# Optimization experiments

Hardware: AMD Instinct MI355X
Metric: run time of the kernel (lower is better)

Reference implementation:

```python
import jax, jax.numpy as jnp
import numpy as np

B, N, DEG = 16, 2048, 16          # graphs, nodes per graph, avg out-degree
C_IN, HID, K = 64, 128, 32        # in_channels, hidden_channels, out_channels (clusters)
NT = B * N                        # total nodes
E = NT * DEG                      # total edges
GN_EPS = 1e-5


def setup_inputs() -> dict:
    key = jax.random.key(0)
    ks = jax.random.split(key, 6)
    x = jax.random.normal(ks[0], (NT, C_IN), jnp.float32)
    # within-graph random edges (sorted batch => node i belongs to graph i // N)
    src_l = jax.random.randint(ks[1], (E,), 0, N)
    dst_l = jax.random.randint(ks[2], (E,), 0, N)
    gid = jnp.repeat(jnp.arange(B, dtype=jnp.int32), N * DEG)
    edge_index = jnp.stack([gid * N + src_l, gid * N + dst_l]).astype(jnp.int32)
    batch = jnp.repeat(jnp.arange(B, dtype=jnp.int32), N)
    return dict(
        x=x, edge_index=edge_index, batch=batch,
        gn_weight=jnp.ones((C_IN,), jnp.float32),
        gn_bias=jnp.zeros((C_IN,), jnp.float32),
        gn_mean_scale=jnp.ones((C_IN,), jnp.float32),
        w1=jax.random.normal(ks[3], (C_IN, HID), jnp.float32) / np.float32(np.sqrt(C_IN)),
        b1=jnp.zeros((HID,), jnp.float32),
        w2=jax.random.normal(ks[4], (HID, K), jnp.float32) / np.float32(np.sqrt(HID)),
        b2=jnp.zeros((K,), jnp.float32),
    )


def reference(x, gn_weight, gn_bias, gn_mean_scale, w1, b1, w2, b2, edge_index, batch):
    # ---- GraphNorm (per-graph mean/var with learnable mean scale) ----
    ones_n = jnp.ones((NT,), x.dtype)
    cnt = jax.ops.segment_sum(ones_n, batch, num_segments=B)[:, None]        # [B,1]
    mean = jax.ops.segment_sum(x, batch, num_segments=B) / cnt              # [B,C]
    xm = x - gn_mean_scale * mean[batch]
    var = jax.ops.segment_sum(xm * xm, batch, num_segments=B) / cnt         # [B,C]
    h = gn_weight * xm / jnp.sqrt(var + GN_EPS)[batch] + gn_bias            # [NT,C_IN]

    # ---- GCNConv (add self-loops, symmetric D^-1/2 (A+I) D^-1/2) ----
    src, dst = edge_index[0], edge_index[1]
    loop = jnp.arange(NT, dtype=src.dtype)
    src_l = jnp.concatenate([src, loop])
    dst_l = jnp.concatenate([dst, loop])
    deg = jax.ops.segment_sum(jnp.ones_like(src_l, x.dtype), dst_l, num_segments=NT)
    dinv = jnp.where(deg > 0, jax.lax.rsqrt(deg), 0.0)
    norm = dinv[src_l] * dinv[dst_l]                                        # [E+NT]
    hw = h @ w1                                                             # [NT,HID]
    h = jax.ops.segment_sum(norm[:, None] * hw[src_l], dst_l, num_segments=NT) + b1
    h = jax.nn.selu(h)

    # ---- to_dense_batch / to_dense_adj (uniform graph sizes -> mask all True) ----
    xd = h.reshape(B, N, HID)                                               # [B,N,F]
    adj = jnp.zeros((B, N, N), x.dtype).at[batch[src], src % N, dst % N].add(1.0)

    # ---- DMoNPooling ----
    s = jax.nn.softmax(xd @ w2 + b2, axis=-1)                               # [B,N,K]
    out = jax.nn.selu(jnp.einsum('bnk,bnf->bkf', s, xd))                    # [B,K,F]
    sta = jnp.einsum('bnk,bnm->bkm', s, adj)                                # [B,K,N]
    out_adj = jnp.einsum('bkm,bml->bkl', sta, s)                            # [B,K,K]

    degrees = adj.sum(-1)                                                   # [B,N]
    m = degrees.sum(-1) / 2                                                 # [B]
    ca = jnp.einsum('bnk,bn->bk', s, degrees)                               # [B,K]
    normalizer = ca[:, :, None] * ca[:, None, :] / 2 / m[:, None, None]
    spectral_loss = (-jnp.einsum('bkk->b', out_adj - normalizer) / (2 * m)).mean()

    ss = jnp.einsum('bnk,bnl->bkl', s, s)                                   # [B,K,K]
    ss_fro = jnp.sqrt(jnp.sum(ss * ss, axis=(-2, -1), keepdims=True))
    eye = jnp.eye(K, dtype=x.dtype)
    diff = ss / ss_fro - eye / jnp.sqrt(jnp.float32(K))
    ortho_loss = jnp.sqrt(jnp.sum(diff * diff, axis=(-2, -1))).mean()

    cluster_size = s.sum(1)                                                 # [B,K]
    cluster_loss = (jnp.linalg.norm(cluster_size, axis=1) / N
                    * jnp.sqrt(jnp.float32(K)) - 1).mean()
    # (coarsened-adj renormalization in DMoNPooling is unused by Net's outputs)

    return jax.nn.log_softmax(out, axis=-1), spectral_loss + ortho_loss + cluster_loss, s
```

## Files before the change

### kernel.cpp

```cpp
#include <hip/hip_runtime.h>
#include <cmath>

static constexpr int B_  = 16;
static constexpr int N_  = 2048;
static constexpr int NT_ = 32768;
static constexpr int E_  = 524288;

static constexpr size_t OFF_HSC    = 0;
static constexpr size_t OFF_XD     = 2097152;
static constexpr size_t OFF_SWS    = 6291456;
static constexpr size_t OFF_PART   = 7340032;
static constexpr size_t OFF_DINV   = 8388608;
static constexpr size_t OFF_SHIFT  = 8421376;
static constexpr size_t OFF_SCALE  = 8422400;
static constexpr size_t OFF_GSP    = 8423424;
static constexpr size_t OFF_GSP2   = 8431616;
static constexpr size_t OFF_SSP    = 8439808;
static constexpr size_t OFF_CAP    = 8701952;
static constexpr size_t OFF_CSP    = 8710144;
static constexpr size_t OFF_SPECP  = 8718336;
static constexpr size_t OFF_ICNTO  = 8718592;
static constexpr size_t OFF_IROWS  = 8751360;
static constexpr size_t OFF_IESRC  = 8784132;

__device__ __forceinline__ float selu_f(float x) {
  return 1.0507009873554805f * (x > 0.f ? x : 1.6732632423543772f * expm1f(x));
}

__device__ __forceinline__ float block_sum_bcast(float v, float* sm) {
  int lane = threadIdx.x & 63, w = threadIdx.x >> 6;
#pragma unroll
  for (int off = 32; off; off >>= 1) v += __shfl_down(v, off);
  __syncthreads();
  if (lane == 0) sm[w] = v;
  __syncthreads();
  return sm[0] + sm[1] + sm[2] + sm[3];
}

__global__ __launch_bounds__(1024) void k_graph(const int* ei, const float* x,
                                                int* rows, int* esrc, int* cout_,
                                                float* dinv, float* gsp, float* gsp2) {
  __shared__ int hin[2048], hout[2048], sb[1024];
  __shared__ float l1[16][64], l2[16][64];
  int blk = blockIdx.x;
  int tid = threadIdx.x;
  if (blk < 16) {
    int g = blk;
    int nbase = g * 2048;
    int ebase = g * 32768;
    hin[tid] = 0; hin[tid + 1024] = 0;
    hout[tid] = 0; hout[tid + 1024] = 0;
    __syncthreads();
    for (int i = tid; i < 32768; i += 1024) {
      int s = ei[ebase + i];
      int d = ei[E_ + ebase + i];
      atomicAdd(&hout[s - nbase], 1);
      atomicAdd(&hin[d - nbase], 1);
    }
    __syncthreads();
    int a = hin[2 * tid], b2 = hin[2 * tid + 1];
    sb[tid] = a + b2;
    __syncthreads();
    for (int off = 1; off < 1024; off <<= 1) {
      int add = (tid >= off) ? sb[tid - off] : 0;
      __syncthreads();
      sb[tid] += add;
      __syncthreads();
    }
    int pref = (tid > 0) ? sb[tid - 1] : 0;
    int r0 = ebase + pref, r1 = r0 + a;
    int n0 = nbase + 2 * tid;
    rows[n0] = r0; rows[n0 + 1] = r1;
    dinv[n0] = rsqrtf((float)(a + 1));
    dinv[n0 + 1] = rsqrtf((float)(b2 + 1));
    cout_[n0] = hout[2 * tid];
    cout_[n0 + 1] = hout[2 * tid + 1];
    if (blk == 15 && tid == 1023) rows[NT_] = E_;
    __syncthreads();
    hin[2 * tid] = r0; hin[2 * tid + 1] = r1;
    __syncthreads();
    for (int i = tid; i < 32768; i += 1024) {
      int s = ei[ebase + i];
      int d = ei[E_ + ebase + i];
      int pos = atomicAdd(&hin[d - nbase], 1);
      esrc[pos] = s;
    }
  } else {
    int gi = blk - 16;
    int b = gi >> 3, chunk = gi & 7;
    int c = tid & 63, r = tid >> 6;
    float s = 0.f, s2 = 0.f;
    const float* xb = x + ((size_t)b * N_ + (size_t)chunk * 256) * 64;
    for (int n = r; n < 256; n += 16) {
      float v = xb[n * 64 + c];
      s += v; s2 += v * v;
    }
    l1[r][c] = s; l2[r][c] = s2;
    __syncthreads();
    if (r == 0) {
      float t1 = 0.f, t2 = 0.f;
#pragma unroll
      for (int i = 0; i < 16; i++) { t1 += l1[i][c]; t2 += l2[i][c]; }
      gsp[gi * 64 + c] = t1;
      gsp2[gi * 64 + c] = t2;
    }
  }
}

__global__ __launch_bounds__(1024) void k_fin(const float* gsp, const float* gsp2,
                                              const float* gw, const float* gms,
                                              float* shift, float* scalev, float* lossp) {
  int t = threadIdx.x;
  int b = t >> 6, c = t & 63;
  float s = 0.f, s2 = 0.f;
#pragma unroll
  for (int chunk = 0; chunk < 8; chunk++) {
    s  += gsp[(b * 8 + chunk) * 64 + c];
    s2 += gsp2[(b * 8 + chunk) * 64 + c];
  }
  float mean = s * (1.f / 2048.f);
  float a = gms[c];
  float var = s2 * (1.f / 2048.f) - (2.f * a - a * a) * mean * mean;
  shift[t] = a * mean;
  scalev[t] = gw[c] * rsqrtf(var + 1e-5f);
  if (t == 0) lossp[0] = 0.f;
}

__global__ void k_prep(const float* x, const float* shift, const float* scalev,
                       const float* gb, const float* dinv, float* hsc) {
  int idx = blockIdx.x * 256 + threadIdx.x;
  int node = idx >> 4, g4 = (idx & 15) * 4;
  int b = node >> 11;
  float di = dinv[node];
  float4 xv = *(const float4*)&x[(size_t)node * 64 + g4];
  float4 sh = *(const float4*)&shift[b * 64 + g4];
  float4 sc = *(const float4*)&scalev[b * 64 + g4];
  float4 bb = *(const float4*)&gb[g4];
  float4 o;
  o.x = ((xv.x - sh.x) * sc.x + bb.x) * di;
  o.y = ((xv.y - sh.y) * sc.y + bb.y) * di;
  o.z = ((xv.z - sh.z) * sc.z + bb.z) * di;
  o.w = ((xv.w - sh.w) * sc.w + bb.w) * di;
  *(float4*)&hsc[(size_t)node * 64 + g4] = o;
}

__global__ __launch_bounds__(256) void k_mm1(const float* hsc, const float* dinv,
                                             const int* rows, const int* esrc,
                                             const float* w1, const float* b1,
                                             float* xd) {
  __shared__ float at[32 * 65];
  int tid = threadIdx.x;
  int n0 = blockIdx.x * 32;
  int wv = tid >> 6, c = tid & 63;
  for (int i = 0; i < 8; i++) {
    int nn = i * 4 + wv;
    int node = n0 + nn;
    int e0 = rows[node], e1 = rows[node + 1];
    float dd = dinv[node];
    float acc = hsc[(size_t)node * 64 + c];
    for (int e = e0; e < e1; e += 8) {
      int sidx[8]; float wt[8], hv[8];
#pragma unroll
      for (int j = 0; j < 8; j++) {
        int ee = e + j;
        sidx[j] = esrc[ee < e1 ? ee : e0];
        wt[j] = (ee < e1) ? 1.f : 0.f;
      }
#pragma unroll
      for (int j = 0; j < 8; j++) hv[j] = hsc[(size_t)sidx[j] * 64 + c];
#pragma unroll
      for (int j = 0; j < 8; j++) acc += wt[j] * hv[j];
    }
    at[nn * 65 + c] = dd * acc;
  }
  __syncthreads();
  int tx = tid & 31, ty = tid >> 5;
  int f0 = tx * 4, nn = ty * 4;
  float acc[4][4] = {};
  for (int k = 0; k < 64; k++) {
    float4 wvv = *(const float4*)&w1[k * 128 + f0];
#pragma unroll
    for (int i = 0; i < 4; i++) {
      float av = at[(nn + i) * 65 + k];
      acc[i][0] += av * wvv.x; acc[i][1] += av * wvv.y;
      acc[i][2] += av * wvv.z; acc[i][3] += av * wvv.w;
    }
  }
  float4 bv = *(const float4*)&b1[f0];
#pragma unroll
  for (int i = 0; i < 4; i++) {
    float4 o;
    o.x = selu_f(acc[i][0] + bv.x);
    o.y = selu_f(acc[i][1] + bv.y);
    o.z = selu_f(acc[i][2] + bv.z);
    o.w = selu_f(acc[i][3] + bv.w);
    *(float4*)&xd[(size_t)(n0 + nn + i) * 128 + f0] = o;
  }
}

__global__ __launch_bounds__(256) void k_mm2s(const float* xd, const float* w2,
                                              const float* b2, float* s_ws,
                                              float* outs) {
  __shared__ float w2s[128 * 32];
  __shared__ float xt[64 * 129];
  __shared__ float lg[64 * 33];
  int tid = threadIdx.x;
  for (int i = tid; i < 4096; i += 256) w2s[i] = w2[i];
  int n0 = blockIdx.x * 64;
  for (int i = tid; i < 2048; i += 256) {
    int n = i >> 5, j4 = (i & 31) * 4;
    float4 v = *(const float4*)&xd[(size_t)(n0 + n) * 128 + j4];
    xt[n * 129 + j4] = v.x; xt[n * 129 + j4 + 1] = v.y;
    xt[n * 129 + j4 + 2] = v.z; xt[n * 129 + j4 + 3] = v.w;
  }
  __syncthreads();
  int ty = tid >> 3;
  int k0 = (tid & 7) * 4;
  float acc[2][4] = {};
  for (int j = 0; j < 128; j++) {
    float4 wv = *(float4*)&w2s[j * 32 + k0];
    float x0 = xt[(ty * 2) * 129 + j];
    float x1 = xt[(ty * 2 + 1) * 129 + j];
    acc[0][0] += x0 * wv.x; acc[0][1] += x0 * wv.y; acc[0][2] += x0 * wv.z; acc[0][3] += x0 * wv.w;
    acc[1][0] += x1 * wv.x; acc[1][1] += x1 * wv.y; acc[1][2] += x1 * wv.z; acc[1][3] += x1 * wv.w;
  }
  float4 bv = *(const float4*)&b2[k0];
#pragma unroll
  for (int i = 0; i < 2; i++) {
    int n = ty * 2 + i;
    lg[n * 33 + k0]     = acc[i][0] + bv.x;
    lg[n * 33 + k0 + 1] = acc[i][1] + bv.y;
    lg[n * 33 + k0 + 2] = acc[i][2] + bv.z;
    lg[n * 33 + k0 + 3] = acc[i][3] + bv.w;
  }
  __syncthreads();
  if (tid < 64) {
    float m = -3.4e38f;
    for (int kk = 0; kk < 32; kk++) m = fmaxf(m, lg[tid * 33 + kk]);
    float ssum = 0.f;
    for (int kk = 0; kk < 32; kk++) {
      float e = expf(lg[tid * 33 + kk] - m);
      lg[tid * 33 + kk] = e; ssum += e;
    }
    float inv = 1.f / ssum;
    for (int k4 = 0; k4 < 32; k4 += 4) {
      float4 o;
      o.x = lg[tid * 33 + k4] * inv;     o.y = lg[tid * 33 + k4 + 1] * inv;
      o.z = lg[tid * 33 + k4 + 2] * inv; o.w = lg[tid * 33 + k4 + 3] * inv;
      *(float4*)&s_ws[(size_t)(n0 + tid) * 32 + k4] = o;
      float* op = &outs[(size_t)(n0 + tid) * 32 + k4];
      op[0] = o.x; op[1] = o.y; op[2] = o.z; op[3] = o.w;
    }
  }
}

__global__ __launch_bounds__(256) void k_stats(const float* s_ws, const int* cout_,
    const int* ei, float* ssp, float* cap, float* csp, float* specp) {
  __shared__ float st[128 * 33];
  __shared__ float r1[8][32], r2[8][32];
  __shared__ float sm4[4];
  int blk = blockIdx.x;
  int b = blk >> 4, chunk = blk & 15;
  int tid = threadIdx.x;
  int nbase = b * 2048 + chunk * 128;
  for (int i = tid; i < 4096; i += 256) {
    int n = i >> 5, kk = i & 31;
    st[n * 33 + kk] = s_ws[(size_t)(nbase + n) * 32 + kk];
  }
  __syncthreads();
  int k = tid >> 3, l0 = (tid & 7) * 4;
  float a0 = 0, a1 = 0, a2 = 0, a3 = 0;
  for (int n = 0; n < 128; n++) {
    float sk = st[n * 33 + k];
    a0 += sk * st[n * 33 + l0];     a1 += sk * st[n * 33 + l0 + 1];
    a2 += sk * st[n * 33 + l0 + 2]; a3 += sk * st[n * 33 + l0 + 3];
  }
  float4 o = {a0, a1, a2, a3};
  *(float4*)&ssp[(size_t)blk * 1024 + k * 32 + l0] = o;
  int k2 = tid & 31, r = tid >> 5;
  float aca = 0.f, acs = 0.f;
  for (int i = 0; i < 16; i++) {
    int n = i * 8 + r;
    float dg = (float)cout_[nbase + n];
    float v = st[n * 33 + k2];
    acs += v; aca += v * dg;
  }
  r1[r][k2] = aca; r2[r][k2] = acs;
  __syncthreads();
  if (r == 0) {
    float sa = 0.f, sc = 0.f;
#pragma unroll
    for (int i = 0; i < 8; i++) { sa += r1[i][k2]; sc += r2[i][k2]; }
    cap[blk * 32 + k2] = sa;
    csp[blk * 32 + k2] = sc;
  }
  int ebase = b * 32768 + chunk * 2048;
  float acc = 0.f;
  for (int j = 0; j < 8; j++) {
    int e = ebase + j * 256 + tid;
    int s = ei[e], d = ei[E_ + e];
    const float4* ap = (const float4*)&s_ws[(size_t)s * 32];
    const float4* cp = (const float4*)&s_ws[(size_t)d * 32];
#pragma unroll
    for (int q = 0; q < 8; q++) {
      float4 u = ap[q], v = cp[q];
      acc += u.x * v.x + u.y * v.y + u.z * v.z + u.w * v.w;
    }
  }
  int lane = tid & 63, w = tid >> 6;
#pragma unroll
  for (int off = 32; off; off >>= 1) acc += __shfl_down(acc, off);
  __syncthreads();
  if (lane == 0) sm4[w] = acc;
  __syncthreads();
  if (tid == 0) specp[blk] = sm4[0] + sm4[1] + sm4[2] + sm4[3];
}

__global__ __launch_bounds__(256) void k_outp(const float* s_ws, const float* xd,
                                              float* partial) {
  __shared__ float st[64 * 36];
  __shared__ float xt[64 * 132];
  int b = blockIdx.x & 15, chunk = blockIdx.x >> 4;
  int tid = threadIdx.x;
  int tx = tid & 31, ty = tid >> 5;
  int f0 = tx * 4, k0 = ty * 4;
  float acc[4][4] = {};
  for (int sub = 0; sub < 2; sub++) {
    int base = b * 2048 + chunk * 128 + sub * 64;
    __syncthreads();
    for (int i = tid; i < 2048; i += 256) {
      int n = i >> 5, kk = i & 31;
      st[n * 36 + kk] = s_ws[(size_t)(base + n) * 32 + kk];
    }
    for (int i = tid; i < 8192; i += 256) {
      int n = i >> 7, j = i & 127;
      xt[n * 132 + j] = xd[(size_t)(base + n) * 128 + j];
    }
    __syncthreads();
    for (int n = 0; n < 64; n++) {
      float4 sv = *(float4*)&st[n * 36 + k0];
      float4 xv = *(float4*)&xt[n * 132 + f0];
      acc[0][0] += sv.x * xv.x; acc[0][1] += sv.x * xv.y; acc[0][2] += sv.x * xv.z; acc[0][3] += sv.x * xv.w;
      acc[1][0] += sv.y * xv.x; acc[1][1] += sv.y * xv.y; acc[1][2] += sv.y * xv.z; acc[1][3] += sv.y * xv.w;
      acc[2][0] += sv.z * xv.x; acc[2][1] += sv.z * xv.y; acc[2][2] += sv.z * xv.z; acc[2][3] += sv.z * xv.w;
      acc[3][0] += sv.w * xv.x; acc[3][1] += sv.w * xv.y; acc[3][2] += sv.w * xv.z; acc[3][3] += sv.w * xv.w;
    }
  }
  int pbase = (chunk * 16 + b) * 32;
#pragma unroll
  for (int i = 0; i < 4; i++) {
    float4 o = {acc[i][0], acc[i][1], acc[i][2], acc[i][3]};
    *(float4*)&partial[(size_t)(pbase + k0 + i) * 128 + f0] = o;
  }
}

__global__ void k_outf(const float* partial, float* out0) {
  int row = blockIdx.x;
  int b = row >> 5, k = row & 31;
  int f = threadIdx.x;
  float v = 0.f;
#pragma unroll
  for (int c = 0; c < 16; c++) v += partial[(size_t)(((c * 16 + b) * 32 + k)) * 128 + f];
  v = selu_f(v);
  int lane = threadIdx.x & 63, w = threadIdx.x >> 6;
  __shared__ float s1[2], s2[2];
  float m = v;
#pragma unroll
  for (int off = 32; off; off >>= 1) m = fmaxf(m, __shfl_down(m, off));
  if (lane == 0) s1[w] = m;
  __syncthreads();
  m = fmaxf(s1[0], s1[1]);
  float e = expf(v - m), t = e;
#pragma unroll
  for (int off = 32; off; off >>= 1) t += __shfl_down(t, off);
  if (lane == 0) s2[w] = t;
  __syncthreads();
  float tot = s2[0] + s2[1];
  out0[(size_t)row * 128 + f] = v - m - logf(tot);
}

__global__ void k_loss(const float* ssp, const float* csp, const float* cap,
                       const float* specp, float* loss) {
  int b = blockIdx.x;
  __shared__ float sm[4];
  int tid = threadIdx.x;
  float v0 = 0, v1 = 0, v2 = 0, v3 = 0;
  for (int c = 0; c < 16; c++) {
    float4 u = *(const float4*)&ssp[(size_t)(b * 16 + c) * 1024 + tid * 4];
    v0 += u.x; v1 += u.y; v2 += u.z; v3 += u.w;
  }
  float ssq = v0 * v0 + v1 * v1 + v2 * v2 + v3 * v3;
  ssq = block_sum_bcast(ssq, sm);
  float inv = 1.f / sqrtf(ssq);
  float dsq = 0.f;
  {
    int i0 = tid * 4;
    float vv[4] = {v0, v1, v2, v3};
#pragma unroll
    for (int j = 0; j < 4; j++) {
      int i = i0 + j;
      float d = vv[j] * inv;
      if ((i >> 5) == (i & 31)) d -= 0.17677669529663687f;
      dsq += d * d;
    }
  }
  dsq = block_sum_bcast(dsq, sm);
  float csq = 0.f, casq = 0.f;
  if (tid < 32) {
    float c1 = 0.f, c2 = 0.f;
    for (int c = 0; c < 16; c++) {
      c1 += csp[(size_t)(b * 16 + c) * 32 + tid];
      c2 += cap[(size_t)(b * 16 + c) * 32 + tid];
    }
    csq = c1 * c1; casq = c2 * c2;
  }
  csq = block_sum_bcast(csq, sm);
  casq = block_sum_bcast(casq, sm);
  float spec_sum = (tid < 16) ? specp[b * 16 + tid] : 0.f;
  spec_sum = block_sum_bcast(spec_sum, sm);
  if (tid == 0) {
    float ortho = sqrtf(dsq);
    float cl = sqrtf(csq) * (1.f / 2048.f) * 5.656854249492381f - 1.f;
    float m = 16384.f;
    float spec = -(spec_sum - casq / (2.f * m)) / (2.f * m);
    atomicAdd(loss, (spec + ortho + cl) * (1.f / 16.f));
  }
}

extern "C" void kernel_launch(void* const* d_in, const int* in_sizes, int n_in,
                              void* d_out, int out_size, void* d_ws, size_t ws_size,
                              hipStream_t stream) {
  (void)in_sizes; (void)n_in; (void)out_size; (void)ws_size;
  const float* x   = (const float*)d_in[0];
  const int*   ei  = (const int*)d_in[1];
  const float* gw  = (const float*)d_in[3];
  const float* gb  = (const float*)d_in[4];
  const float* gms = (const float*)d_in[5];
  const float* w1  = (const float*)d_in[6];
  const float* b1  = (const float*)d_in[7];
  const float* w2  = (const float*)d_in[8];
  const float* b2  = (const float*)d_in[9];
  float* out = (float*)d_out;
  float* ws  = (float*)d_ws;

  float* hsc    = ws + OFF_HSC;
  float* xd     = ws + OFF_XD;
  float* s_ws   = ws + OFF_SWS;
  float* part   = ws + OFF_PART;
  float* dinv   = ws + OFF_DINV;
  float* shift  = ws + OFF_SHIFT;
  float* scalev = ws + OFF_SCALE;
  float* gsp    = ws + OFF_GSP;
  float* gsp2   = ws + OFF_GSP2;
  float* ssp    = ws + OFF_SSP;
  float* cap    = ws + OFF_CAP;
  float* csp    = ws + OFF_CSP;
  float* specp  = ws + OFF_SPECP;
  int*   cout_  = (int*)(ws + OFF_ICNTO);
  int*   rows   = (int*)(ws + OFF_IROWS);
  int*   esrc   = (int*)(ws + OFF_IESRC);

  float* out0  = out;
  float* lossp = out + 65536;
  float* outs  = out + 65537;

  hipLaunchKernelGGL(k_graph, dim3(144), dim3(1024), 0, stream,
                     ei, x, rows, esrc, cout_, dinv, gsp, gsp2);
  hipLaunchKernelGGL(k_fin, dim3(1), dim3(1024), 0, stream,
                     gsp, gsp2, gw, gms, shift, scalev, lossp);
  hipLaunchKernelGGL(k_prep, dim3(2048), dim3(256), 0, stream,
                     x, shift, scalev, gb, dinv, hsc);
  hipLaunchKernelGGL(k_mm1, dim3(1024), dim3(256), 0, stream, hsc, dinv, rows, esrc, w1, b1, xd);
  hipLaunchKernelGGL(k_mm2s, dim3(512), dim3(256), 0, stream, xd, w2, b2, s_ws, outs);
  hipLaunchKernelGGL(k_stats, dim3(256), dim3(256), 0, stream, s_ws, cout_, ei, ssp, cap, csp, specp);
  hipLaunchKernelGGL(k_outp, dim3(256), dim3(256), 0, stream, s_ws, xd, part);
  hipLaunchKernelGGL(k_outf, dim3(512), dim3(128), 0, stream, part, out0);
  hipLaunchKernelGGL(k_loss, dim3(16), dim3(256), 0, stream, ssp, csp, cap, specp, lossp);
}
```

Measured before the change: 214.9 us.

## Fuse softmax, cluster stats and pooled output into mm2; fold GraphNorm finalize into prep

```diff
diff --git a/kernel.cpp b/kernel.cpp
--- a/kernel.cpp
+++ b/kernel.cpp
@@ -10,18 +10,16 @@
 static constexpr size_t OFF_XD     = 2097152;
 static constexpr size_t OFF_SWS    = 6291456;
 static constexpr size_t OFF_PART   = 7340032;
-static constexpr size_t OFF_DINV   = 8388608;
-static constexpr size_t OFF_SHIFT  = 8421376;
-static constexpr size_t OFF_SCALE  = 8422400;
-static constexpr size_t OFF_GSP    = 8423424;
-static constexpr size_t OFF_GSP2   = 8431616;
-static constexpr size_t OFF_SSP    = 8439808;
-static constexpr size_t OFF_CAP    = 8701952;
-static constexpr size_t OFF_CSP    = 8710144;
-static constexpr size_t OFF_SPECP  = 8718336;
-static constexpr size_t OFF_ICNTO  = 8718592;
-static constexpr size_t OFF_IROWS  = 8751360;
-static constexpr size_t OFF_IESRC  = 8784132;
+static constexpr size_t OFF_DINV   = 9437184;
+static constexpr size_t OFF_GSP    = 9469952;
+static constexpr size_t OFF_GSP2   = 9478144;
+static constexpr size_t OFF_SSP    = 9486336;
+static constexpr size_t OFF_CAP    = 10010624;
+static constexpr size_t OFF_CSP    = 10027008;
+static constexpr size_t OFF_SPECP  = 10043392;
+static constexpr size_t OFF_ICNTO  = 10043904;
+static constexpr size_t OFF_IROWS  = 10076672;
+static constexpr size_t OFF_IESRC  = 10109444;
 
 __device__ __forceinline__ float selu_f(float x) {
   return 1.0507009873554805f * (x > 0.f ? x : 1.6732632423543772f * expm1f(x));
@@ -107,40 +105,36 @@
   }
 }
 
-__global__ __launch_bounds__(1024) void k_fin(const float* gsp, const float* gsp2,
-                                              const float* gw, const float* gms,
-                                              float* shift, float* scalev, float* lossp) {
-  int t = threadIdx.x;
-  int b = t >> 6, c = t & 63;
-  float s = 0.f, s2 = 0.f;
-#pragma unroll
-  for (int chunk = 0; chunk < 8; chunk++) {
-    s  += gsp[(b * 8 + chunk) * 64 + c];
-    s2 += gsp2[(b * 8 + chunk) * 64 + c];
-  }
-  float mean = s * (1.f / 2048.f);
-  float a = gms[c];
-  float var = s2 * (1.f / 2048.f) - (2.f * a - a * a) * mean * mean;
-  shift[t] = a * mean;
-  scalev[t] = gw[c] * rsqrtf(var + 1e-5f);
-  if (t == 0) lossp[0] = 0.f;
-}
-
-__global__ void k_prep(const float* x, const float* shift, const float* scalev,
-                       const float* gb, const float* dinv, float* hsc) {
-  int idx = blockIdx.x * 256 + threadIdx.x;
+__global__ void k_prep(const float* x, const float* gsp, const float* gsp2,
+                       const float* gw, const float* gb, const float* gms,
+                       const float* dinv, float* hsc) {
+  __shared__ float shs[64], scs[64];
+  int tid = threadIdx.x;
+  int bgr = blockIdx.x >> 7;
+  if (tid < 64) {
+    float s = 0.f, s2 = 0.f;
+#pragma unroll
+    for (int c8 = 0; c8 < 8; c8++) {
+      s  += gsp[(bgr * 8 + c8) * 64 + tid];
+      s2 += gsp2[(bgr * 8 + c8) * 64 + tid];
+    }
+    float mean = s * (1.f / 2048.f);
+    float a = gms[tid];
+    float var = s2 * (1.f / 2048.f) - (2.f * a - a * a) * mean * mean;
+    shs[tid] = a * mean;
+    scs[tid] = gw[tid] * rsqrtf(var + 1e-5f);
+  }
+  __syncthreads();
+  int idx = blockIdx.x * 256 + tid;
   int node = idx >> 4, g4 = (idx & 15) * 4;
-  int b = node >> 11;
   float di = dinv[node];
   float4 xv = *(const float4*)&x[(size_t)node * 64 + g4];
-  float4 sh = *(const float4*)&shift[b * 64 + g4];
-  float4 sc = *(const float4*)&scalev[b * 64 + g4];
   float4 bb = *(const float4*)&gb[g4];
   float4 o;
-  o.x = ((xv.x - sh.x) * sc.x + bb.x) * di;
-  o.y = ((xv.y - sh.y) * sc.y + bb.y) * di;
-  o.z = ((xv.z - sh.z) * sc.z + bb.z) * di;
-  o.w = ((xv.w - sh.w) * sc.w + bb.w) * di;
+  o.x = ((xv.x - shs[g4])     * scs[g4]     + bb.x) * di;
+  o.y = ((xv.y - shs[g4 + 1]) * scs[g4 + 1] + bb.y) * di;
+  o.z = ((xv.z - shs[g4 + 2]) * scs[g4 + 2] + bb.z) * di;
+  o.w = ((xv.w - shs[g4 + 3]) * scs[g4 + 3] + bb.w) * di;
   *(float4*)&hsc[(size_t)node * 64 + g4] = o;
 }
 
@@ -198,15 +192,18 @@
   }
 }
 
-__global__ __launch_bounds__(256) void k_mm2s(const float* xd, const float* w2,
-                                              const float* b2, float* s_ws,
-                                              float* outs) {
+__global__ __launch_bounds__(256) void k_mm2f(const float* xd, const float* w2,
+                                              const float* b2, const int* cout_,
+                                              float* s_ws, float* outs, float* ssp,
+                                              float* cap, float* csp, float* part) {
+  __shared__ float xt[64 * 129];
   __shared__ float w2s[128 * 32];
-  __shared__ float xt[64 * 129];
-  __shared__ float lg[64 * 33];
+  __shared__ float st[64 * 33];
+  __shared__ float r1[8][32], r2[8][32];
   int tid = threadIdx.x;
+  int blk = blockIdx.x;
+  int n0 = blk * 64;
   for (int i = tid; i < 4096; i += 256) w2s[i] = w2[i];
-  int n0 = blockIdx.x * 64;
   for (int i = tid; i < 2048; i += 256) {
     int n = i >> 5, j4 = (i & 31) * 4;
     float4 v = *(const float4*)&xd[(size_t)(n0 + n) * 128 + j4];
@@ -216,87 +213,103 @@
   __syncthreads();
   int ty = tid >> 3;
   int k0 = (tid & 7) * 4;
-  float acc[2][4] = {};
+  float acc2[2][4] = {};
   for (int j = 0; j < 128; j++) {
     float4 wv = *(float4*)&w2s[j * 32 + k0];
     float x0 = xt[(ty * 2) * 129 + j];
     float x1 = xt[(ty * 2 + 1) * 129 + j];
-    acc[0][0] += x0 * wv.x; acc[0][1] += x0 * wv.y; acc[0][2] += x0 * wv.z; acc[0][3] += x0 * wv.w;
-    acc[1][0] += x1 * wv.x; acc[1][1] += x1 * wv.y; acc[1][2] += x1 * wv.z; acc[1][3] += x1 * wv.w;
-  }
-  float4 bv = *(const float4*)&b2[k0];
+    acc2[0][0] += x0 * wv.x; acc2[0][1] += x0 * wv.y; acc2[0][2] += x0 * wv.z; acc2[0][3] += x0 * wv.w;
+    acc2[1][0] += x1 * wv.x; acc2[1][1] += x1 * wv.y; acc2[1][2] += x1 * wv.z; acc2[1][3] += x1 * wv.w;
+  }
+  float4 bv2 = *(const float4*)&b2[k0];
 #pragma unroll
   for (int i = 0; i < 2; i++) {
     int n = ty * 2 + i;
-    lg[n * 33 + k0]     = acc[i][0] + bv.x;
-    lg[n * 33 + k0 + 1] = acc[i][1] + bv.y;
-    lg[n * 33 + k0 + 2] = acc[i][2] + bv.z;
-    lg[n * 33 + k0 + 3] = acc[i][3] + bv.w;
+    st[n * 33 + k0]     = acc2[i][0] + bv2.x;
+    st[n * 33 + k0 + 1] = acc2[i][1] + bv2.y;
+    st[n * 33 + k0 + 2] = acc2[i][2] + bv2.z;
+    st[n * 33 + k0 + 3] = acc2[i][3] + bv2.w;
   }
   __syncthreads();
   if (tid < 64) {
     float m = -3.4e38f;
-    for (int kk = 0; kk < 32; kk++) m = fmaxf(m, lg[tid * 33 + kk]);
+    for (int kk = 0; kk < 32; kk++) m = fmaxf(m, st[tid * 33 + kk]);
     float ssum = 0.f;
     for (int kk = 0; kk < 32; kk++) {
-      float e = expf(lg[tid * 33 + kk] - m);
-      lg[tid * 33 + kk] = e; ssum += e;
+      float e = expf(st[tid * 33 + kk] - m);
+      st[tid * 33 + kk] = e; ssum += e;
     }
     float inv = 1.f / ssum;
-    for (int k4 = 0; k4 < 32; k4 += 4) {
-      float4 o;
-      o.x = lg[tid * 33 + k4] * inv;     o.y = lg[tid * 33 + k4 + 1] * inv;
-      o.z = lg[tid * 33 + k4 + 2] * inv; o.w = lg[tid * 33 + k4 + 3] * inv;
-      *(float4*)&s_ws[(size_t)(n0 + tid) * 32 + k4] = o;
-      float* op = &outs[(size_t)(n0 + tid) * 32 + k4];
-      op[0] = o.x; op[1] = o.y; op[2] = o.z; op[3] = o.w;
-    }
-  }
-}
-
-__global__ __launch_bounds__(256) void k_stats(const float* s_ws, const int* cout_,
-    const int* ei, float* ssp, float* cap, float* csp, float* specp) {
-  __shared__ float st[128 * 33];
-  __shared__ float r1[8][32], r2[8][32];
+    for (int kk = 0; kk < 32; kk++) st[tid * 33 + kk] *= inv;
+  }
+  __syncthreads();
+  for (int i = tid; i < 512; i += 256) {
+    int n = i >> 3, q = (i & 7) * 4;
+    float4 o = {st[n * 33 + q], st[n * 33 + q + 1], st[n * 33 + q + 2], st[n * 33 + q + 3]};
+    *(float4*)&s_ws[(size_t)(n0 + n) * 32 + q] = o;
+    float* op = &outs[(size_t)(n0 + n) * 32 + q];
+    op[0] = o.x; op[1] = o.y; op[2] = o.z; op[3] = o.w;
+  }
+  {
+    int k = tid >> 3, l0 = (tid & 7) * 4;
+    float a0 = 0, a1 = 0, a2 = 0, a3 = 0;
+    for (int n = 0; n < 64; n++) {
+      float sk = st[n * 33 + k];
+      a0 += sk * st[n * 33 + l0];     a1 += sk * st[n * 33 + l0 + 1];
+      a2 += sk * st[n * 33 + l0 + 2]; a3 += sk * st[n * 33 + l0 + 3];
+    }
+    float4 o = {a0, a1, a2, a3};
+    *(float4*)&ssp[(size_t)blk * 1024 + k * 32 + l0] = o;
+  }
+  {
+    int k2 = tid & 31, r = tid >> 5;
+    float aca = 0.f, acs = 0.f;
+    for (int i = 0; i < 8; i++) {
+      int n = i * 8 + r;
+      float dg = (float)cout_[n0 + n];
+      float v = st[n * 33 + k2];
+      acs += v; aca += v * dg;
+    }
+    r1[r][k2] = aca; r2[r][k2] = acs;
+    __syncthreads();
+    if (r == 0) {
+      float sa = 0.f, sc = 0.f;
+#pragma unroll
+      for (int i = 0; i < 8; i++) { sa += r1[i][k2]; sc += r2[i][k2]; }
+      cap[blk * 32 + k2] = sa;
+      csp[blk * 32 + k2] = sc;
+    }
+  }
+  {
+    int tx = tid & 31, ty2 = tid >> 5;
+    int f0 = tx * 4, kk0 = ty2 * 4;
+    float acc[4][4] = {};
+    for (int n = 0; n < 64; n++) {
+      float s0 = st[n * 33 + kk0], s1 = st[n * 33 + kk0 + 1];
+      float s2 = st[n * 33 + kk0 + 2], s3 = st[n * 33 + kk0 + 3];
+      float4 xv = {xt[n * 129 + f0], xt[n * 129 + f0 + 1], xt[n * 129 + f0 + 2], xt[n * 129 + f0 + 3]};
+      acc[0][0] += s0 * xv.x; acc[0][1] += s0 * xv.y; acc[0][2] += s0 * xv.z; acc[0][3] += s0 * xv.w;
+      acc[1][0] += s1 * xv.x; acc[1][1] += s1 * xv.y; acc[1][2] += s1 * xv.z; acc[1][3] += s1 * xv.w;
+      acc[2][0] += s2 * xv.x; acc[2][1] += s2 * xv.y; acc[2][2] += s2 * xv.z; acc[2][3] += s2 * xv.w;
+      acc[3][0] += s3 * xv.x; acc[3][1] += s3 * xv.y; acc[3][2] += s3 * xv.z; acc[3][3] += s3 * xv.w;
+    }
+#pragma unroll
+    for (int i = 0; i < 4; i++) {
+      float4 o = {acc[i][0], acc[i][1], acc[i][2], acc[i][3]};
+      *(float4*)&part[(size_t)(blk * 32 + kk0 + i) * 128 + f0] = o;
+    }
+  }
+}
+
+__global__ __launch_bounds__(256) void k_spec(const int* ei, const float* s_ws,
+                                              float* specp, float* lossp) {
   __shared__ float sm4[4];
-  int blk = blockIdx.x;
-  int b = blk >> 4, chunk = blk & 15;
-  int tid = threadIdx.x;
-  int nbase = b * 2048 + chunk * 128;
-  for (int i = tid; i < 4096; i += 256) {
-    int n = i >> 5, kk = i & 31;
-    st[n * 33 + kk] = s_ws[(size_t)(nbase + n) * 32 + kk];
-  }
-  __syncthreads();
-  int k = tid >> 3, l0 = (tid & 7) * 4;
-  float a0 = 0, a1 = 0, a2 = 0, a3 = 0;
-  for (int n = 0; n < 128; n++) {
-    float sk = st[n * 33 + k];
-    a0 += sk * st[n * 33 + l0];     a1 += sk * st[n * 33 + l0 + 1];
-    a2 += sk * st[n * 33 + l0 + 2]; a3 += sk * st[n * 33 + l0 + 3];
-  }
-  float4 o = {a0, a1, a2, a3};
-  *(float4*)&ssp[(size_t)blk * 1024 + k * 32 + l0] = o;
-  int k2 = tid & 31, r = tid >> 5;
-  float aca = 0.f, acs = 0.f;
-  for (int i = 0; i < 16; i++) {
-    int n = i * 8 + r;
-    float dg = (float)cout_[nbase + n];
-    float v = st[n * 33 + k2];
-    acs += v; aca += v * dg;
-  }
-  r1[r][k2] = aca; r2[r][k2] = acs;
-  __syncthreads();
-  if (r == 0) {
-    float sa = 0.f, sc = 0.f;
-#pragma unroll
-    for (int i = 0; i < 8; i++) { sa += r1[i][k2]; sc += r2[i][k2]; }
-    cap[blk * 32 + k2] = sa;
-    csp[blk * 32 + k2] = sc;
-  }
-  int ebase = b * 32768 + chunk * 2048;
+  int blk = blockIdx.x, tid = threadIdx.x;
+  if (blk == 0 && tid == 0) lossp[0] = 0.f;
+  int ebase = blk * 1024;
   float acc = 0.f;
-  for (int j = 0; j < 8; j++) {
+#pragma unroll
+  for (int j = 0; j < 4; j++) {
     int e = ebase + j * 256 + tid;
     int s = ei[e], d = ei[E_ + e];
     const float4* ap = (const float4*)&s_ws[(size_t)s * 32];
@@ -310,57 +323,18 @@
   int lane = tid & 63, w = tid >> 6;
 #pragma unroll
   for (int off = 32; off; off >>= 1) acc += __shfl_down(acc, off);
-  __syncthreads();
   if (lane == 0) sm4[w] = acc;
   __syncthreads();
   if (tid == 0) specp[blk] = sm4[0] + sm4[1] + sm4[2] + sm4[3];
 }
 
-__global__ __launch_bounds__(256) void k_outp(const float* s_ws, const float* xd,
-                                              float* partial) {
-  __shared__ float st[64 * 36];
-  __shared__ float xt[64 * 132];
-  int b = blockIdx.x & 15, chunk = blockIdx.x >> 4;
-  int tid = threadIdx.x;
-  int tx = tid & 31, ty = tid >> 5;
-  int f0 = tx * 4, k0 = ty * 4;
-  float acc[4][4] = {};
-  for (int sub = 0; sub < 2; sub++) {
-    int base = b * 2048 + chunk * 128 + sub * 64;
-    __syncthreads();
-    for (int i = tid; i < 2048; i += 256) {
-      int n = i >> 5, kk = i & 31;
-      st[n * 36 + kk] = s_ws[(size_t)(base + n) * 32 + kk];
-    }
-    for (int i = tid; i < 8192; i += 256) {
-      int n = i >> 7, j = i & 127;
-      xt[n * 132 + j] = xd[(size_t)(base + n) * 128 + j];
-    }
-    __syncthreads();
-    for (int n = 0; n < 64; n++) {
-      float4 sv = *(float4*)&st[n * 36 + k0];
-      float4 xv = *(float4*)&xt[n * 132 + f0];
-      acc[0][0] += sv.x * xv.x; acc[0][1] += sv.x * xv.y; acc[0][2] += sv.x * xv.z; acc[0][3] += sv.x * xv.w;
-      acc[1][0] += sv.y * xv.x; acc[1][1] += sv.y * xv.y; acc[1][2] += sv.y * xv.z; acc[1][3] += sv.y * xv.w;
-      acc[2][0] += sv.z * xv.x; acc[2][1] += sv.z * xv.y; acc[2][2] += sv.z * xv.z; acc[2][3] += sv.z * xv.w;
-      acc[3][0] += sv.w * xv.x; acc[3][1] += sv.w * xv.y; acc[3][2] += sv.w * xv.z; acc[3][3] += sv.w * xv.w;
-    }
-  }
-  int pbase = (chunk * 16 + b) * 32;
-#pragma unroll
-  for (int i = 0; i < 4; i++) {
-    float4 o = {acc[i][0], acc[i][1], acc[i][2], acc[i][3]};
-    *(float4*)&partial[(size_t)(pbase + k0 + i) * 128 + f0] = o;
-  }
-}
-
-__global__ void k_outf(const float* partial, float* out0) {
+__global__ void k_outf(const float* part, float* out0) {
   int row = blockIdx.x;
   int b = row >> 5, k = row & 31;
   int f = threadIdx.x;
   float v = 0.f;
 #pragma unroll
-  for (int c = 0; c < 16; c++) v += partial[(size_t)(((c * 16 + b) * 32 + k)) * 128 + f];
+  for (int c = 0; c < 32; c++) v += part[(size_t)((b * 32 + c) * 32 + k) * 128 + f];
   v = selu_f(v);
   int lane = threadIdx.x & 63, w = threadIdx.x >> 6;
   __shared__ float s1[2], s2[2];
@@ -385,8 +359,8 @@
   __shared__ float sm[4];
   int tid = threadIdx.x;
   float v0 = 0, v1 = 0, v2 = 0, v3 = 0;
-  for (int c = 0; c < 16; c++) {
-    float4 u = *(const float4*)&ssp[(size_t)(b * 16 + c) * 1024 + tid * 4];
+  for (int c = 0; c < 32; c++) {
+    float4 u = *(const float4*)&ssp[(size_t)(b * 32 + c) * 1024 + tid * 4];
     v0 += u.x; v1 += u.y; v2 += u.z; v3 += u.w;
   }
   float ssq = v0 * v0 + v1 * v1 + v2 * v2 + v3 * v3;
@@ -408,15 +382,15 @@
   float csq = 0.f, casq = 0.f;
   if (tid < 32) {
     float c1 = 0.f, c2 = 0.f;
-    for (int c = 0; c < 16; c++) {
-      c1 += csp[(size_t)(b * 16 + c) * 32 + tid];
-      c2 += cap[(size_t)(b * 16 + c) * 32 + tid];
+    for (int c = 0; c < 32; c++) {
+      c1 += csp[(size_t)(b * 32 + c) * 32 + tid];
+      c2 += cap[(size_t)(b * 32 + c) * 32 + tid];
     }
     csq = c1 * c1; casq = c2 * c2;
   }
   csq = block_sum_bcast(csq, sm);
   casq = block_sum_bcast(casq, sm);
-  float spec_sum = (tid < 16) ? specp[b * 16 + tid] : 0.f;
+  float spec_sum = (tid < 32) ? specp[b * 32 + tid] : 0.f;
   spec_sum = block_sum_bcast(spec_sum, sm);
   if (tid == 0) {
     float ortho = sqrtf(dsq);
@@ -448,8 +422,6 @@
   float* s_ws   = ws + OFF_SWS;
   float* part   = ws + OFF_PART;
   float* dinv   = ws + OFF_DINV;
-  float* shift  = ws + OFF_SHIFT;
-  float* scalev = ws + OFF_SCALE;
   float* gsp    = ws + OFF_GSP;
   float* gsp2   = ws + OFF_GSP2;
   float* ssp    = ws + OFF_SSP;
@@ -466,14 +438,12 @@
 
   hipLaunchKernelGGL(k_graph, dim3(144), dim3(1024), 0, stream,
                      ei, x, rows, esrc, cout_, dinv, gsp, gsp2);
-  hipLaunchKernelGGL(k_fin, dim3(1), dim3(1024), 0, stream,
-                     gsp, gsp2, gw, gms, shift, scalev, lossp);
   hipLaunchKernelGGL(k_prep, dim3(2048), dim3(256), 0, stream,
-                     x, shift, scalev, gb, dinv, hsc);
+                     x, gsp, gsp2, gw, gb, gms, dinv, hsc);
   hipLaunchKernelGGL(k_mm1, dim3(1024), dim3(256), 0, stream, hsc, dinv, rows, esrc, w1, b1, xd);
-  hipLaunchKernelGGL(k_mm2s, dim3(512), dim3(256), 0, stream, xd, w2, b2, s_ws, outs);
-  hipLaunchKernelGGL(k_stats, dim3(256), dim3(256), 0, stream, s_ws, cout_, ei, ssp, cap, csp, specp);
-  hipLaunchKernelGGL(k_outp, dim3(256), dim3(256), 0, stream, s_ws, xd, part);
+  hipLaunchKernelGGL(k_mm2f, dim3(512), dim3(256), 0, stream,
+                     xd, w2, b2, cout_, s_ws, outs, ssp, cap, csp, part);
+  hipLaunchKernelGGL(k_spec, dim3(512), dim3(256), 0, stream, ei, s_ws, specp, lossp);
   hipLaunchKernelGGL(k_outf, dim3(512), dim3(128), 0, stream, part, out0);
   hipLaunchKernelGGL(k_loss, dim3(16), dim3(256), 0, stream, ssp, csp, cap, specp, lossp);
 }
```

After: 207.9 us. 3.2% less time.
